# Performance work log

Hardware: AMD Instinct MI355X
Metric: run time of the kernel (lower is better)

## Reference

```python
import jax, jax.numpy as jnp
import numpy as np

EMBED_DIM = 1024
NUM_HEADS = 16
HEAD_DIM = EMBED_DIM // NUM_HEADS
L = 1024  # target/source seq len
N = 2     # batch
EPS = 1e-6


def setup_inputs() -> dict:
    key = jax.random.key(0)
    ks = jax.random.split(key, 11)
    s = 0.02
    return {
        "query": jax.random.normal(ks[0], (L, N, EMBED_DIM), jnp.float32),
        "key": jax.random.normal(ks[1], (L, N, EMBED_DIM), jnp.float32),
        "value": jax.random.normal(ks[2], (L, N, EMBED_DIM), jnp.float32),
        "Wq": jax.random.normal(ks[3], (EMBED_DIM, EMBED_DIM), jnp.float32) * s,
        "bq": jnp.zeros((EMBED_DIM,), jnp.float32),
        "Wk": jax.random.normal(ks[4], (EMBED_DIM, EMBED_DIM), jnp.float32) * s,
        "bk": jnp.zeros((EMBED_DIM,), jnp.float32),
        "Wv": jax.random.normal(ks[5], (EMBED_DIM, EMBED_DIM), jnp.float32) * s,
        "bv": jnp.zeros((EMBED_DIM,), jnp.float32),
        "Wo": jax.random.normal(ks[6], (EMBED_DIM, EMBED_DIM), jnp.float32) * s,
        "bo": jnp.zeros((EMBED_DIM,), jnp.float32),
    }


def _feature_map(x):
    # phi(x) = elu(x) + 1 (Katharopoulos et al., 2020)
    return jax.nn.elu(x) + 1.0


def reference(query, key, value, Wq, bq, Wk, bk, Wv, bv, Wo, bo):
    tgt_len, bsz, embed_dim = query.shape
    H, d = NUM_HEADS, HEAD_DIM
    # projections (torch Linear: x @ W.T + b)
    q = query @ Wq.T + bq
    k = key @ Wk.T + bk
    v = value @ Wv.T + bv
    # (L, N, E) -> (N*H, L, d)
    def to_heads(x):
        return x.reshape(-1, bsz * H, d).transpose(1, 0, 2)
    q, k, v = to_heads(q), to_heads(k), to_heads(v)
    q = _feature_map(q)
    k = _feature_map(k)
    # causal linear attention: S_t = cumsum_s<=t k_s v_s^T ; z_t = cumsum k_s
    kv = jnp.cumsum(jnp.einsum('bld,ble->blde', k, v), axis=1)  # (B*H, L, d, d)
    num = jnp.einsum('bld,blde->ble', q, kv)                    # (B*H, L, d)
    z = jnp.cumsum(k, axis=1)                                   # (B*H, L, d)
    denom = jnp.einsum('bld,bld->bl', q, z) + EPS               # (B*H, L)
    attn = num / denom[..., None]
    # (N*H, L, d) -> (L, N, E)
    attn = attn.transpose(1, 0, 2).reshape(tgt_len, bsz, embed_dim)
    return attn @ Wo.T + bo
```

## Files before the change

kernel.cpp:

```cpp
#include <hip/hip_runtime.h>
#include <cmath>


#define EPS 1e-6f

typedef short bf16x8 __attribute__((ext_vector_type(8)));
typedef float f32x4 __attribute__((ext_vector_type(4)));

__device__ __forceinline__ float b2f(ushort u) {
    union { unsigned u32; float f; } x; x.u32 = ((unsigned)u) << 16; return x.f;
}
__device__ __forceinline__ ushort f2b(float f) {
    union { float f; unsigned u; } x; x.f = f;
    unsigned r = (x.u + 0x7fffu + ((x.u >> 16) & 1u)) >> 16;
    return (ushort)r;
}
__device__ __forceinline__ void gload16(const void* g, void* l) {
    __builtin_amdgcn_global_load_lds(
        (__attribute__((address_space(1))) void*)(uintptr_t)g,
        (__attribute__((address_space(3))) void*)l,
        16, 0, 0);
}

template<int KSTEPS>
__device__ __forceinline__ void gemm_mainloop6(const ushort* __restrict__ A,
                                               const ushort* __restrict__ B,
                                               int brow, int bcol, int kbeg,
                                               ushort* Sh, f32x4 acc[4][4]) {
    const int K = 1024;
    const int BUFE = 16384;
    int tid = threadIdx.x;
    int w = tid >> 6, lane = tid & 63;
    int fr = lane & 15, hi = lane >> 4;
    int wr = w >> 1, wc = w & 1;

    const ushort* gsrc[8];
    int ldst[8];
    #pragma unroll
    for (int i = 0; i < 8; i++) {
        int s = (w * 8 + i) * 64 + lane;
        const ushort* base; int r, sl;
        if (s < 1024) { r = s >> 3; sl = s & 7; base = A + (size_t)(brow + r) * K; }
        else { int s2 = s - 1024; r = s2 >> 3; sl = s2 & 7; base = B + (size_t)(bcol + r) * K; }
        gsrc[i] = base + kbeg + ((sl ^ (r & 7)) * 8);
        ldst[i] = (w * 8 + i) * 512;
    }

    int ea[4][2], eb[4][2];
    #pragma unroll
    for (int m = 0; m < 4; m++) {
        int ra = wr * 64 + m * 16 + fr;
        #pragma unroll
        for (int kk = 0; kk < 2; kk++)
            ea[m][kk] = ra * 64 + (((hi + kk * 4) ^ (ra & 7)) * 8);
    }
    #pragma unroll
    for (int n = 0; n < 4; n++) {
        int rb = wc * 64 + n * 16 + fr;
        #pragma unroll
        for (int kk = 0; kk < 2; kk++)
            eb[n][kk] = 8192 + rb * 64 + (((hi + kk * 4) ^ (rb & 7)) * 8);
    }

    #pragma unroll
    for (int m = 0; m < 4; m++)
        #pragma unroll
        for (int n = 0; n < 4; n++)
            acc[m][n] = (f32x4){0.f, 0.f, 0.f, 0.f};

    #pragma unroll
    for (int i = 0; i < 8; i++) gload16(gsrc[i], Sh + ldst[i]);
    __syncthreads();

    for (int t = 0; t < KSTEPS; ++t) {
        if (t + 1 < KSTEPS) {
            ushort* Sn = Sh + ((t + 1) & 1) * BUFE;
            #pragma unroll
            for (int i = 0; i < 8; i++) gload16(gsrc[i] + (t + 1) * 64, Sn + ldst[i]);
        }
        const ushort* Bc = Sh + (t & 1) * BUFE;
        #pragma unroll
        for (int kk = 0; kk < 2; kk++) {
            bf16x8 af[4], bf[4];
            #pragma unroll
            for (int m = 0; m < 4; m++) af[m] = *(const bf16x8*)&Bc[ea[m][kk]];
            #pragma unroll
            for (int n = 0; n < 4; n++) bf[n] = *(const bf16x8*)&Bc[eb[n][kk]];
            #pragma unroll
            for (int m = 0; m < 4; m++)
                #pragma unroll
                for (int n = 0; n < 4; n++)
                    acc[m][n] = __builtin_amdgcn_mfma_f32_16x16x32_bf16(af[m], bf[n], acc[m][n], 0, 0, 0);
        }
        __syncthreads();
    }
}

__global__ __launch_bounds__(256, 2) void gemm_proj(
    const ushort* __restrict__ Aq, const ushort* __restrict__ Ak, const ushort* __restrict__ Av,
    const ushort* __restrict__ Bq, const ushort* __restrict__ Bk, const ushort* __restrict__ Bv,
    const float* __restrict__ bq, const float* __restrict__ bk, const float* __restrict__ bv,
    ushort* __restrict__ oq, ushort* __restrict__ ok, ushort* __restrict__ ov) {
    __shared__ ushort Sh[2 * 16384];
    int bid = blockIdx.x;
    int swz = (bid & 7) * 48 + (bid >> 3);
    int z = swz >> 7;
    int rem = swz & 127;
    int brow = (rem >> 3) * 128, bcol = (rem & 7) * 128;
    const ushort* A = (z == 0) ? Aq : (z == 1) ? Ak : Av;
    const ushort* B = (z == 0) ? Bq : (z == 1) ? Bk : Bv;
    const float* bias = (z == 0) ? bq : (z == 1) ? bk : bv;
    f32x4 acc[4][4];
    gemm_mainloop6<16>(A, B, brow, bcol, 0, Sh, acc);
    int tid = threadIdx.x, w = tid >> 6, lane = tid & 63;
    int fr = lane & 15, hi = lane >> 4;
    int wr = w >> 1, wc = w & 1;
    #pragma unroll
    for (int m = 0; m < 4; m++)
        #pragma unroll
        for (int n = 0; n < 4; n++)
            #pragma unroll
            for (int r = 0; r < 4; r++) {
                int grow = brow + wr * 64 + m * 16 + hi * 4 + r;
                int gcol = bcol + wc * 64 + n * 16 + fr;
                float v = acc[m][n][r] + bias[gcol];
                int l = grow >> 1, nb2 = grow & 1, h = gcol >> 6, dd = gcol & 63;
                if (z == 2) {
                    ov[(size_t)((nb2 * 16 + h) * 64 + dd) * 1024 + l] = f2b(v);
                } else {
                    v = (v > 0.f) ? v + 1.f : __expf(v);
                    ushort* out = (z == 0) ? oq : ok;
                    out[(size_t)((nb2 * 16 + h) * 1024 + l) * 64 + dd] = f2b(v);
                }
            }
}

__global__ __launch_bounds__(256, 2) void gemm_outk(const ushort* __restrict__ A,
                                                    const ushort* __restrict__ B,
                                                    float* __restrict__ pbuf) {
    __shared__ ushort Sh[2 * 16384];
    int bid = blockIdx.x;
    int swz = (bid & 7) * 32 + (bid >> 3);
    int z = swz >> 7;
    int rem = swz & 127;
    int brow = (rem >> 3) * 128, bcol = (rem & 7) * 128;
    f32x4 acc[4][4];
    gemm_mainloop6<8>(A, B, brow, bcol, z * 512, Sh, acc);
    int tid = threadIdx.x, w = tid >> 6, lane = tid & 63;
    int fr = lane & 15, hi = lane >> 4;
    int wr = w >> 1, wc = w & 1;
    float* out = pbuf + (size_t)z * 2097152;
    #pragma unroll
    for (int m = 0; m < 4; m++)
        #pragma unroll
        for (int n = 0; n < 4; n++)
            #pragma unroll
            for (int r = 0; r < 4; r++) {
                int grow = brow + wr * 64 + m * 16 + hi * 4 + r;
                int gcol = bcol + wc * 64 + n * 16 + fr;
                out[(size_t)grow * 1024 + gcol] = acc[m][n][r];
            }
}

__global__ __launch_bounds__(256) void reduce_out(const float* __restrict__ p,
                                                  const float* __restrict__ bias,
                                                  float* __restrict__ out) {
    int i = blockIdx.x * 256 + threadIdx.x;
    float4 a = ((const float4*)p)[i];
    float4 b = ((const float4*)(p + 2097152))[i];
    float4 bb = ((const float4*)bias)[i & 255];
    float4 o;
    o.x = a.x + b.x + bb.x;
    o.y = a.y + b.y + bb.y;
    o.z = a.z + b.z + bb.z;
    o.w = a.w + b.w + bb.w;
    ((float4*)out)[i] = o;
}

__global__ __launch_bounds__(256) void cast_all(
    const float* __restrict__ i0, const float* __restrict__ i1, const float* __restrict__ i2,
    const float* __restrict__ i3, const float* __restrict__ i4, const float* __restrict__ i5,
    const float* __restrict__ i6,
    ushort* __restrict__ o0, ushort* __restrict__ o1, ushort* __restrict__ o2,
    ushort* __restrict__ o3, ushort* __restrict__ o4, ushort* __restrict__ o5,
    ushort* __restrict__ o6) {
    int z = blockIdx.z;
    const float* in = (z == 0) ? i0 : (z == 1) ? i1 : (z == 2) ? i2 :
                      (z == 3) ? i3 : (z == 4) ? i4 : (z == 5) ? i5 : i6;
    ushort* out = (z == 0) ? o0 : (z == 1) ? o1 : (z == 2) ? o2 :
                  (z == 3) ? o3 : (z == 4) ? o4 : (z == 5) ? o5 : o6;
    int n4 = (z < 3) ? 524288 : 262144;
    int i = blockIdx.x * 256 + threadIdx.x;
    if (i < n4) {
        float4 f = ((const float4*)in)[i];
        ushort4 o; o.x = f2b(f.x); o.y = f2b(f.y); o.z = f2b(f.z); o.w = f2b(f.w);
        ((ushort4*)out)[i] = o;
    }
}

__global__ __launch_bounds__(256) void chunk_sums(const ushort* __restrict__ kh,
                                                  const ushort* __restrict__ vt,
                                                  float* __restrict__ St,
                                                  float* __restrict__ zc) {
    int c = blockIdx.x, b = blockIdx.y, tid = threadIdx.x;
    __shared__ float Kl[64][64];
    __shared__ float Vl[64][65];
    const ushort* Kg = kh + (size_t)(b * 1024 + c * 64) * 64;
    for (int i = tid; i < 1024; i += 256) {
        ushort4 k4 = ((const ushort4*)Kg)[i];
        ((float4*)Kl)[i] = make_float4(b2f(k4.x), b2f(k4.y), b2f(k4.z), b2f(k4.w));
        int e = i >> 4, s4 = (i & 15) << 2;
        ushort4 v4 = *(const ushort4*)&vt[(size_t)(b * 64 + e) * 1024 + c * 64 + s4];
        Vl[e][s4 + 0] = b2f(v4.x); Vl[e][s4 + 1] = b2f(v4.y);
        Vl[e][s4 + 2] = b2f(v4.z); Vl[e][s4 + 3] = b2f(v4.w);
    }
    __syncthreads();
    int e = tid & 63, d0 = (tid >> 6) * 16;
    float s[16] = {};
    for (int ss = 0; ss < 64; ss++) {
        float ve = Vl[e][ss];
        #pragma unroll
        for (int i = 0; i < 16; i++) s[i] += Kl[ss][d0 + i] * ve;
    }
    float* So = St + (size_t)(b * 16 + c) * 4096 + e * 64 + d0;
    #pragma unroll
    for (int k = 0; k < 4; k++)
        *(float4*)&So[k * 4] = make_float4(s[4*k], s[4*k+1], s[4*k+2], s[4*k+3]);
    if (tid < 64) {
        float z = 0.f;
        for (int ss = 0; ss < 64; ss++) z += Kl[ss][tid];
        zc[(size_t)(b * 16 + c) * 64 + tid] = z;
    }
}

__global__ __launch_bounds__(256) void prefix_chunks(const float* __restrict__ St,
                                                     ushort* __restrict__ Spt,
                                                     float* __restrict__ zc) {
    int b = blockIdx.x, tid = threadIdx.x;
    size_t base = (size_t)b * 16 * 4096 + (size_t)tid * 16;
    float run[16] = {};
    for (int c = 0; c < 16; c++) {
        const float4* p4 = (const float4*)(St + base + (size_t)c * 4096);
        ushort* q = Spt + base + (size_t)c * 4096;
        #pragma unroll
        for (int k = 0; k < 4; k++) {
            float4 v = p4[k];
            ushort4 o;
            o.x = f2b(run[4*k+0]); o.y = f2b(run[4*k+1]);
            o.z = f2b(run[4*k+2]); o.w = f2b(run[4*k+3]);
            ((ushort4*)q)[k] = o;
            run[4*k+0] += v.x; run[4*k+1] += v.y; run[4*k+2] += v.z; run[4*k+3] += v.w;
        }
    }
    if (tid < 64) {
        float rz = 0.f;
        for (int c = 0; c < 16; c++) {
            size_t idx = ((size_t)b * 16 + c) * 64 + tid;
            float t = zc[idx];
            zc[idx] = rz;
            rz += t;
        }
    }
}

__global__ __launch_bounds__(256) void attn_chunk(const ushort* __restrict__ qh,
                                                  const ushort* __restrict__ kh,
                                                  const ushort* __restrict__ vt,
                                                  const ushort* __restrict__ Spt,
                                                  const float* __restrict__ zc,
                                                  ushort* __restrict__ attn) {
    int c = blockIdx.x, b = blockIdx.y, tid = threadIdx.x;
    int w = tid >> 6, lane = tid & 63;
    int fr = lane & 15, hi = lane >> 4;
    __shared__ ushort Q[4096], Kt[4096], VT[4096], SP[4096], P[4096];
    __shared__ float den[64];

    {
        const ushort* bases[4];
        bases[0] = qh + (size_t)(b * 1024 + c * 64) * 64;
        bases[1] = kh + (size_t)(b * 1024 + c * 64) * 64;
        bases[2] = vt;
        bases[3] = Spt + (size_t)(b * 16 + c) * 4096;
        ushort* dsts[4] = {Q, Kt, VT, SP};
        #pragma unroll
        for (int tl = 0; tl < 4; tl++) {
            #pragma unroll
            for (int j = 0; j < 2; j++) {
                int i = w * 64 + lane + 256 * j;
                int row = i >> 3, sl = i & 7;
                int col = (sl ^ (row & 7)) * 8;
                const ushort* src;
                if (tl == 2) src = vt + (size_t)(b * 64 + row) * 1024 + c * 64 + col;
                else         src = bases[tl] + (size_t)row * 64 + col;
                gload16(src, dsts[tl] + w * 512 + 2048 * j);
            }
        }
    }
    __syncthreads();

    int frow = w * 16 + fr;
    int fkey = fr & 7;
    bf16x8 aq[2];
    #pragma unroll
    for (int kk = 0; kk < 2; kk++)
        aq[kk] = *(const bf16x8*)&Q[frow * 64 + ((kk * 4 + hi) ^ fkey) * 8];
    f32x4 pc[4];
    #pragma unroll
    for (int n = 0; n < 4; n++) {
        pc[n] = (f32x4){0.f, 0.f, 0.f, 0.f};
        #pragma unroll
        for (int kk = 0; kk < 2; kk++) {
            bf16x8 bk_ = *(const bf16x8*)&Kt[(n * 16 + fr) * 64 + ((kk * 4 + hi) ^ fkey) * 8];
            pc[n] = __builtin_amdgcn_mfma_f32_16x16x32_bf16(aq[kk], bk_, pc[n], 0, 0, 0);
        }
    }
    float denp[4] = {0.f, 0.f, 0.f, 0.f};
    #pragma unroll
    for (int n = 0; n < 4; n++)
        #pragma unroll
        for (int r = 0; r < 4; r++) {
            int t = w * 16 + hi * 4 + r;
            int s = n * 16 + fr;
            float v = (s <= t) ? pc[n][r] : 0.f;
            denp[r] += v;
            P[t * 64 + (((s >> 3) ^ (t & 7)) * 8) + (s & 7)] = f2b(v);
        }
    #pragma unroll
    for (int r = 0; r < 4; r++) {
        denp[r] += __shfl_xor(denp[r], 1);
        denp[r] += __shfl_xor(denp[r], 2);
        denp[r] += __shfl_xor(denp[r], 4);
        denp[r] += __shfl_xor(denp[r], 8);
    }
    if (fr == 0) {
        #pragma unroll
        for (int r = 0; r < 4; r++) den[w * 16 + hi * 4 + r] = denp[r];
    }
    __syncthreads();

    if (tid < 64) {
        int t = tid;
        const float* zg = zc + (size_t)(b * 16 + c) * 64;
        float a = 0.f;
        for (int d = 0; d < 64; d++)
            a += b2f(Q[t * 64 + (((d >> 3) ^ (t & 7)) * 8) + (d & 7)]) * zg[d];
        den[t] += a;
    }

    bf16x8 ap[2];
    #pragma unroll
    for (int kk = 0; kk < 2; kk++)
        ap[kk] = *(const bf16x8*)&P[frow * 64 + ((kk * 4 + hi) ^ fkey) * 8];
    f32x4 nacc[4];
    #pragma unroll
    for (int n = 0; n < 4; n++) {
        nacc[n] = (f32x4){0.f, 0.f, 0.f, 0.f};
        #pragma unroll
        for (int kk = 0; kk < 2; kk++) {
            bf16x8 bs = *(const bf16x8*)&SP[(n * 16 + fr) * 64 + ((kk * 4 + hi) ^ fkey) * 8];
            nacc[n] = __builtin_amdgcn_mfma_f32_16x16x32_bf16(aq[kk], bs, nacc[n], 0, 0, 0);
        }
        #pragma unroll
        for (int kk = 0; kk < 2; kk++) {
            bf16x8 bv = *(const bf16x8*)&VT[(n * 16 + fr) * 64 + ((kk * 4 + hi) ^ fkey) * 8];
            nacc[n] = __builtin_amdgcn_mfma_f32_16x16x32_bf16(ap[kk], bv, nacc[n], 0, 0, 0);
        }
    }
    __syncthreads();

    int nb = b >> 4, h = b & 15;
    #pragma unroll
    for (int n = 0; n < 4; n++)
        #pragma unroll
        for (int r = 0; r < 4; r++) {
            int t = w * 16 + hi * 4 + r;
            int e = n * 16 + fr;
            int l = c * 64 + t;
            float val = nacc[n][r] / (den[t] + EPS);
            attn[(size_t)(l * 2 + nb) * 1024 + h * 64 + e] = f2b(val);
        }
}

extern "C" void kernel_launch(void* const* d_in, const int* in_sizes, int n_in,
                              void* d_out, int out_size, void* d_ws, size_t ws_size,
                              hipStream_t stream) {
    const float* query = (const float*)d_in[0];
    const float* key_  = (const float*)d_in[1];
    const float* value = (const float*)d_in[2];
    const float* Wq = (const float*)d_in[3];
    const float* bq = (const float*)d_in[4];
    const float* Wk = (const float*)d_in[5];
    const float* bk = (const float*)d_in[6];
    const float* Wv = (const float*)d_in[7];
    const float* bv = (const float*)d_in[8];
    const float* Wo = (const float*)d_in[9];
    const float* bo = (const float*)d_in[10];

    ushort* qbuf = (ushort*)d_ws;
    ushort* kbuf = qbuf + 2097152;
    ushort* vbuf = kbuf + 2097152;
    ushort* wqb  = vbuf + 2097152;
    ushort* wkb  = wqb + 1048576;
    ushort* wvb  = wkb + 1048576;
    ushort* wob  = wvb + 1048576;
    ushort* qh   = wob + 1048576;
    ushort* kh   = qh + 2097152;
    ushort* vt   = kh + 2097152;
    float*  St   = (float*)(vt + 2097152);
    ushort* Spt  = (ushort*)(St + 2097152);
    float*  zc   = (float*)(Spt + 2097152);
    float*  pbuf = zc + 32768;
    ushort* attn = qbuf;

    cast_all<<<dim3(2048, 1, 7), 256, 0, stream>>>(query, key_, value, Wq, Wk, Wv, Wo,
                                                   qbuf, kbuf, vbuf, wqb, wkb, wvb, wob);

    gemm_proj<<<384, 256, 0, stream>>>(qbuf, kbuf, vbuf, wqb, wkb, wvb,
                                       bq, bk, bv, qh, kh, vt);

    chunk_sums<<<dim3(16, 32), 256, 0, stream>>>(kh, vt, St, zc);
    prefix_chunks<<<32, 256, 0, stream>>>(St, Spt, zc);
    attn_chunk<<<dim3(16, 32), 256, 0, stream>>>(qh, kh, vt, Spt, zc, attn);

    gemm_outk<<<256, 256, 0, stream>>>(attn, wob, pbuf);
    reduce_out<<<2048, 256, 0, stream>>>(pbuf, bo, (float*)d_out);
}
```

Measured before the change: 84.77 us.

## Split GEMM K across two wave groups and widen prefix-scan grid

The projection and output GEMMs now launch 512 threads per block: two groups of four waves each handle half of the K range. Each group loads its own 32-column K slice per step and reduces partial accumulators through shared memory at the end. The goal is more waves per block to hide MFMA and LDS latency. The cost is the extra reduction and only half the threads doing the epilogue. Separately, the chunk prefix scan is spread over four times as many blocks, with each thread handling four elements instead of sixteen, to raise parallelism.

```diff
diff --git a/kernel.cpp b/kernel.cpp
--- a/kernel.cpp
+++ b/kernel.cpp
@@ -23,7 +23,7 @@
 }
 
 template<int KSTEPS>
-__device__ __forceinline__ void gemm_mainloop6(const ushort* __restrict__ A,
+__device__ __forceinline__ void gemm_mainloop7(const ushort* __restrict__ A,
                                                const ushort* __restrict__ B,
                                                int brow, int bcol, int kbeg,
                                                ushort* Sh, f32x4 acc[4][4]) {
@@ -32,34 +32,33 @@
     int tid = threadIdx.x;
     int w = tid >> 6, lane = tid & 63;
     int fr = lane & 15, hi = lane >> 4;
-    int wr = w >> 1, wc = w & 1;
-
-    const ushort* gsrc[8];
-    int ldst[8];
-    #pragma unroll
-    for (int i = 0; i < 8; i++) {
-        int s = (w * 8 + i) * 64 + lane;
+    int khalf = w >> 2, quad = w & 3;
+    int wr = quad >> 1, wc = quad & 1;
+
+    const ushort* gsrc[4];
+    int ldst[4];
+    #pragma unroll
+    for (int i = 0; i < 4; i++) {
+        int s = (w * 4 + i) * 64 + lane;
         const ushort* base; int r, sl;
         if (s < 1024) { r = s >> 3; sl = s & 7; base = A + (size_t)(brow + r) * K; }
         else { int s2 = s - 1024; r = s2 >> 3; sl = s2 & 7; base = B + (size_t)(bcol + r) * K; }
-        gsrc[i] = base + kbeg + ((sl ^ (r & 7)) * 8);
-        ldst[i] = (w * 8 + i) * 512;
-    }
-
-    int ea[4][2], eb[4][2];
+        int orig = sl ^ (r & 7);
+        int khw = orig >> 2, c16 = orig & 3;
+        gsrc[i] = base + kbeg + khw * (KSTEPS * 32) + c16 * 8;
+        ldst[i] = (w * 4 + i) * 512;
+    }
+
+    int ea[4], eb[4];
     #pragma unroll
     for (int m = 0; m < 4; m++) {
         int ra = wr * 64 + m * 16 + fr;
-        #pragma unroll
-        for (int kk = 0; kk < 2; kk++)
-            ea[m][kk] = ra * 64 + (((hi + kk * 4) ^ (ra & 7)) * 8);
+        ea[m] = ra * 64 + (((khalf * 4 + hi) ^ (ra & 7)) * 8);
     }
     #pragma unroll
     for (int n = 0; n < 4; n++) {
         int rb = wc * 64 + n * 16 + fr;
-        #pragma unroll
-        for (int kk = 0; kk < 2; kk++)
-            eb[n][kk] = 8192 + rb * 64 + (((hi + kk * 4) ^ (rb & 7)) * 8);
+        eb[n] = 8192 + rb * 64 + (((khalf * 4 + hi) ^ (rb & 7)) * 8);
     }
 
     #pragma unroll
@@ -69,34 +68,48 @@
             acc[m][n] = (f32x4){0.f, 0.f, 0.f, 0.f};
 
     #pragma unroll
-    for (int i = 0; i < 8; i++) gload16(gsrc[i], Sh + ldst[i]);
+    for (int i = 0; i < 4; i++) gload16(gsrc[i], Sh + ldst[i]);
     __syncthreads();
 
     for (int t = 0; t < KSTEPS; ++t) {
         if (t + 1 < KSTEPS) {
             ushort* Sn = Sh + ((t + 1) & 1) * BUFE;
             #pragma unroll
-            for (int i = 0; i < 8; i++) gload16(gsrc[i] + (t + 1) * 64, Sn + ldst[i]);
+            for (int i = 0; i < 4; i++) gload16(gsrc[i] + (t + 1) * 32, Sn + ldst[i]);
         }
         const ushort* Bc = Sh + (t & 1) * BUFE;
-        #pragma unroll
-        for (int kk = 0; kk < 2; kk++) {
-            bf16x8 af[4], bf[4];
-            #pragma unroll
-            for (int m = 0; m < 4; m++) af[m] = *(const bf16x8*)&Bc[ea[m][kk]];
-            #pragma unroll
-            for (int n = 0; n < 4; n++) bf[n] = *(const bf16x8*)&Bc[eb[n][kk]];
-            #pragma unroll
-            for (int m = 0; m < 4; m++)
-                #pragma unroll
-                for (int n = 0; n < 4; n++)
-                    acc[m][n] = __builtin_amdgcn_mfma_f32_16x16x32_bf16(af[m], bf[n], acc[m][n], 0, 0, 0);
-        }
+        bf16x8 af[4], bf[4];
+        #pragma unroll
+        for (int m = 0; m < 4; m++) af[m] = *(const bf16x8*)&Bc[ea[m]];
+        #pragma unroll
+        for (int n = 0; n < 4; n++) bf[n] = *(const bf16x8*)&Bc[eb[n]];
+        #pragma unroll
+        for (int m = 0; m < 4; m++)
+            #pragma unroll
+            for (int n = 0; n < 4; n++)
+                acc[m][n] = __builtin_amdgcn_mfma_f32_16x16x32_bf16(af[m], bf[n], acc[m][n], 0, 0, 0);
         __syncthreads();
     }
-}
-
-__global__ __launch_bounds__(256, 2) void gemm_proj(
+
+    float* red = (float*)Sh;
+    if (khalf == 1) {
+        #pragma unroll
+        for (int m = 0; m < 4; m++)
+            #pragma unroll
+            for (int n = 0; n < 4; n++)
+                *(f32x4*)&red[(quad * 16 + m * 4 + n) * 256 + lane * 4] = acc[m][n];
+    }
+    __syncthreads();
+    if (khalf == 0) {
+        #pragma unroll
+        for (int m = 0; m < 4; m++)
+            #pragma unroll
+            for (int n = 0; n < 4; n++)
+                acc[m][n] += *(const f32x4*)&red[(quad * 16 + m * 4 + n) * 256 + lane * 4];
+    }
+}
+
+__global__ __launch_bounds__(512) void gemm_proj(
     const ushort* __restrict__ Aq, const ushort* __restrict__ Ak, const ushort* __restrict__ Av,
     const ushort* __restrict__ Bq, const ushort* __restrict__ Bk, const ushort* __restrict__ Bv,
     const float* __restrict__ bq, const float* __restrict__ bk, const float* __restrict__ bv,
@@ -111,10 +124,11 @@
     const ushort* B = (z == 0) ? Bq : (z == 1) ? Bk : Bv;
     const float* bias = (z == 0) ? bq : (z == 1) ? bk : bv;
     f32x4 acc[4][4];
-    gemm_mainloop6<16>(A, B, brow, bcol, 0, Sh, acc);
+    gemm_mainloop7<16>(A, B, brow, bcol, 0, Sh, acc);
     int tid = threadIdx.x, w = tid >> 6, lane = tid & 63;
+    if (w >= 4) return;
     int fr = lane & 15, hi = lane >> 4;
-    int wr = w >> 1, wc = w & 1;
+    int wr = (w >> 1) & 1, wc = w & 1;
     #pragma unroll
     for (int m = 0; m < 4; m++)
         #pragma unroll
@@ -135,9 +149,9 @@
             }
 }
 
-__global__ __launch_bounds__(256, 2) void gemm_outk(const ushort* __restrict__ A,
-                                                    const ushort* __restrict__ B,
-                                                    float* __restrict__ pbuf) {
+__global__ __launch_bounds__(512) void gemm_outk(const ushort* __restrict__ A,
+                                                 const ushort* __restrict__ B,
+                                                 float* __restrict__ pbuf) {
     __shared__ ushort Sh[2 * 16384];
     int bid = blockIdx.x;
     int swz = (bid & 7) * 32 + (bid >> 3);
@@ -145,10 +159,11 @@
     int rem = swz & 127;
     int brow = (rem >> 3) * 128, bcol = (rem & 7) * 128;
     f32x4 acc[4][4];
-    gemm_mainloop6<8>(A, B, brow, bcol, z * 512, Sh, acc);
+    gemm_mainloop7<8>(A, B, brow, bcol, z * 512, Sh, acc);
     int tid = threadIdx.x, w = tid >> 6, lane = tid & 63;
+    if (w >= 4) return;
     int fr = lane & 15, hi = lane >> 4;
-    int wr = w >> 1, wc = w & 1;
+    int wr = (w >> 1) & 1, wc = w & 1;
     float* out = pbuf + (size_t)z * 2097152;
     #pragma unroll
     for (int m = 0; m < 4; m++)
@@ -236,23 +251,19 @@
 __global__ __launch_bounds__(256) void prefix_chunks(const float* __restrict__ St,
                                                      ushort* __restrict__ Spt,
                                                      float* __restrict__ zc) {
-    int b = blockIdx.x, tid = threadIdx.x;
-    size_t base = (size_t)b * 16 * 4096 + (size_t)tid * 16;
-    float run[16] = {};
+    int b = blockIdx.x, by = blockIdx.y, tid = threadIdx.x;
+    int e = by * 16 + (tid >> 4);
+    int d0 = (tid & 15) * 4;
+    size_t base = (size_t)b * 65536 + (size_t)e * 64 + d0;
+    float run[4] = {};
     for (int c = 0; c < 16; c++) {
-        const float4* p4 = (const float4*)(St + base + (size_t)c * 4096);
-        ushort* q = Spt + base + (size_t)c * 4096;
-        #pragma unroll
-        for (int k = 0; k < 4; k++) {
-            float4 v = p4[k];
-            ushort4 o;
-            o.x = f2b(run[4*k+0]); o.y = f2b(run[4*k+1]);
-            o.z = f2b(run[4*k+2]); o.w = f2b(run[4*k+3]);
-            ((ushort4*)q)[k] = o;
-            run[4*k+0] += v.x; run[4*k+1] += v.y; run[4*k+2] += v.z; run[4*k+3] += v.w;
-        }
-    }
-    if (tid < 64) {
+        float4 v = *(const float4*)&St[base + (size_t)c * 4096];
+        ushort4 o;
+        o.x = f2b(run[0]); o.y = f2b(run[1]); o.z = f2b(run[2]); o.w = f2b(run[3]);
+        *(ushort4*)&Spt[base + (size_t)c * 4096] = o;
+        run[0] += v.x; run[1] += v.y; run[2] += v.z; run[3] += v.w;
+    }
+    if (by == 0 && tid < 64) {
         float rz = 0.f;
         for (int c = 0; c < 16; c++) {
             size_t idx = ((size_t)b * 16 + c) * 64 + tid;
@@ -415,13 +426,13 @@
     cast_all<<<dim3(2048, 1, 7), 256, 0, stream>>>(query, key_, value, Wq, Wk, Wv, Wo,
                                                    qbuf, kbuf, vbuf, wqb, wkb, wvb, wob);
 
-    gemm_proj<<<384, 256, 0, stream>>>(qbuf, kbuf, vbuf, wqb, wkb, wvb,
+    gemm_proj<<<384, 512, 0, stream>>>(qbuf, kbuf, vbuf, wqb, wkb, wvb,
                                        bq, bk, bv, qh, kh, vt);
 
     chunk_sums<<<dim3(16, 32), 256, 0, stream>>>(kh, vt, St, zc);
-    prefix_chunks<<<32, 256, 0, stream>>>(St, Spt, zc);
+    prefix_chunks<<<dim3(32, 4), 256, 0, stream>>>(St, Spt, zc);
     attn_chunk<<<dim3(16, 32), 256, 0, stream>>>(qh, kh, vt, Spt, zc, attn);
 
-    gemm_outk<<<256, 256, 0, stream>>>(attn, wob, pbuf);
+    gemm_outk<<<256, 512, 0, stream>>>(attn, wob, pbuf);
     reduce_out<<<2048, 256, 0, stream>>>(pbuf, bo, (float*)d_out);
 }
```

Result: no change. 85.60 us (+1.0%).
